# Performance work log

Hardware: AMD Instinct MI355X
Metric: run time of the kernel (lower is better)

## Reference

```python
import jax, jax.numpy as jnp
import numpy as np

N = 6720      # 16 graphs * 420 nodes
E = 33600     # 16 graphs * 2100 edges (5 per node)
DIN = 2048
H1, C1 = 2, 1024   # conv1: heads=2, out=1024 -> concat 2048
H2, C2 = 1, 64     # conv2: heads=1, out=64
ED = 64            # edge_dim
NODES_PER_GRAPH = 420


def _lin(k, fi, fo):
    return jax.random.normal(k, (fi, fo), jnp.float32) / np.sqrt(fi).astype(np.float32)


def setup_inputs() -> dict:
    key = jax.random.key(0)
    ks = jax.random.split(key, 24)
    d = {}
    d["x"] = jax.random.normal(ks[0], (N, DIN), jnp.float32)
    d["edge_index"] = jax.random.randint(ks[1], (2, E), 0, N)
    # tiled learned edge_features param (torch.rand init), one 2100xED block per graph
    ef = jax.random.uniform(ks[2], (5 * NODES_PER_GRAPH, ED), jnp.float32)
    d["edge_attr"] = jnp.tile(ef, (N // NODES_PER_GRAPH, 1))
    HC1 = H1 * C1
    d["q1_w"] = _lin(ks[3], DIN, HC1); d["q1_b"] = jax.random.normal(ks[4], (HC1,)) * 0.01
    d["k1_w"] = _lin(ks[5], DIN, HC1); d["k1_b"] = jax.random.normal(ks[6], (HC1,)) * 0.01
    d["v1_w"] = _lin(ks[7], DIN, HC1); d["v1_b"] = jax.random.normal(ks[8], (HC1,)) * 0.01
    d["e1_w"] = _lin(ks[9], ED, HC1)                      # lin_edge has no bias in PyG
    d["s1_w"] = _lin(ks[10], DIN, HC1); d["s1_b"] = jax.random.normal(ks[11], (HC1,)) * 0.01
    HC2 = H2 * C2
    d["q2_w"] = _lin(ks[12], HC1, HC2); d["q2_b"] = jax.random.normal(ks[13], (HC2,)) * 0.01
    d["k2_w"] = _lin(ks[14], HC1, HC2); d["k2_b"] = jax.random.normal(ks[15], (HC2,)) * 0.01
    d["v2_w"] = _lin(ks[16], HC1, HC2); d["v2_b"] = jax.random.normal(ks[17], (HC2,)) * 0.01
    d["e2_w"] = _lin(ks[18], ED, HC2)
    d["s2_w"] = _lin(ks[19], HC1, HC2); d["s2_b"] = jax.random.normal(ks[20], (HC2,)) * 0.01
    return d


def _transformer_conv(x, src, dst, edge_attr, qw, qb, kw, kb, vw, vb, ew, sw, sb, H, C):
    """PyG TransformerConv (concat=True, beta=False, root_weight=True)."""
    n = x.shape[0]
    q = (x @ qw + qb).reshape(n, H, C)
    k = (x @ kw + kb).reshape(n, H, C)
    v = (x @ vw + vb).reshape(n, H, C)
    e = (edge_attr @ ew).reshape(-1, H, C)         # [E,H,C]
    kj = k[src] + e                                # gather source keys + edge emb
    alpha = jnp.sum(q[dst] * kj, axis=-1) / np.sqrt(C).astype(np.float32)  # [E,H]
    # scatter-softmax over incoming edges of each target node
    amax = jax.ops.segment_max(alpha, dst, num_segments=n)   # [N,H]
    ex = jnp.exp(alpha - amax[dst])
    denom = jax.ops.segment_sum(ex, dst, num_segments=n)
    attn = ex / (denom[dst] + 1e-16)               # [E,H]
    msg = (v[src] + e) * attn[..., None]           # [E,H,C]
    out = jax.ops.segment_sum(msg, dst, num_segments=n).reshape(n, H * C)
    return out + x @ sw + sb                       # root/skip connection


def reference(x, edge_index, edge_attr,
              q1_w, q1_b, k1_w, k1_b, v1_w, v1_b, e1_w, s1_w, s1_b,
              q2_w, q2_b, k2_w, k2_b, v2_w, v2_b, e2_w, s2_w, s2_b):
    src, dst = edge_index[0], edge_index[1]
    h = jax.nn.relu(_transformer_conv(x, src, dst, edge_attr,
                                      q1_w, q1_b, k1_w, k1_b, v1_w, v1_b,
                                      e1_w, s1_w, s1_b, H1, C1))
    h = jax.nn.relu(_transformer_conv(h, src, dst, edge_attr,
                                      q2_w, q2_b, k2_w, k2_b, v2_w, v2_b,
                                      e2_w, s2_w, s2_b, H2, C2))
    return h.reshape(-1, NODES_PER_GRAPH * 64)     # forward returns here (fc layers are dead code)
```

## Files before the change

### kernel.cpp

```cpp
#include <hip/hip_runtime.h>
#include <hip/hip_bf16.h>
#include <cstdint>
#include <cstddef>

#define NN    6720
#define MPAD  6912
#define NE    33600
#define KDIM  2048
#define HC1   2048
#define EAP   2100

typedef __attribute__((ext_vector_type(8))) short bhalf8;
typedef __attribute__((ext_vector_type(4))) short bhalf4;
typedef __attribute__((ext_vector_type(4))) float fx4;

__device__ __forceinline__ float bf2f(short s) {
    union { unsigned int u; float f; } c;
    c.u = ((unsigned int)(unsigned short)s) << 16;
    return c.f;
}

__device__ __forceinline__ void gload16(const __hip_bfloat16* g, void* lds)
{
    __builtin_amdgcn_global_load_lds(
        (const __attribute__((address_space(1))) unsigned int*)g,
        (__attribute__((address_space(3))) unsigned int*)lds,
        16, 0, 0);
}

#define CFENCE asm volatile("" ::: "memory")

__global__ __launch_bounds__(512, 2) void gemm256_8ph(
    const __hip_bfloat16* __restrict__ A,
    const __hip_bfloat16* __restrict__ Bt,
    const float* __restrict__ bcat,
    __hip_bfloat16* __restrict__ oq,
    __hip_bfloat16* __restrict__ ok,
    __hip_bfloat16* __restrict__ ov,
    float* __restrict__ oh)
{
    __shared__ alignas(16) char Lds[131072];

    const int bid = blockIdx.x;
    const int i0  = bid >> 3;
    const int bx  = (bid & 7) * 4 + (i0 & 3);
    const int by  = i0 >> 2;

    const int tid  = threadIdx.x;
    const int w    = tid >> 6;
    const int lane = tid & 63;
    const int wm = w >> 2, wn = w & 3;
    const int l15 = lane & 15;
    const int rowA = by * 256;
    const int rowB = bx * 256;

    const int sug = ((lane & 7) ^ (lane >> 3)) << 3;
    const __hip_bfloat16* Agb = A  + (size_t)(rowA + w * 16 + (lane >> 3)) * KDIM + sug;
    const __hip_bfloat16* Bgb = Bt + (size_t)(rowB + w * 16 + (lane >> 3)) * KDIM + sug;

    const int uk0 = (((lane >> 4)    ) ^ (lane & 7)) << 4;
    const int uk1 = (((lane >> 4) + 4) ^ (lane & 7)) << 4;

    fx4 acc[8][4] = {};

#define STAGE_A(T, H)                                                      \
    { char* dst_ = Lds + ((T) & 1) * 32768 + (H) * 16384 + (w * 16) * 128; \
      const __hip_bfloat16* g_ = Agb + (size_t)((H) * 128) * KDIM + (size_t)(T) * 64; \
      gload16(g_, dst_);                                                   \
      gload16(g_ + 8 * KDIM, dst_ + 1024); }

#define STAGE_B(T, H)                                                      \
    { char* dst_ = Lds + 65536 + ((T) & 1) * 32768 + (H) * 16384 + (w * 16) * 128; \
      const __hip_bfloat16* g_ = Bgb + (size_t)((H) * 128) * KDIM + (size_t)(T) * 64; \
      gload16(g_, dst_);                                                   \
      gload16(g_ + 8 * KDIM, dst_ + 1024); }

#define PH_READ_AF(q)                                                      \
    _Pragma("unroll")                                                      \
    for (int m2 = 0; m2 < 2; ++m2) {                                       \
        const char* rp_ = Ab + (((q) * 2 + m2) * 16 + l15) * 128;          \
        af[m2][0] = *(const bhalf8*)(rp_ + uk0);                           \
        af[m2][1] = *(const bhalf8*)(rp_ + uk1);                           \
    }

#define PH_MFMA(q)                                                         \
    __builtin_amdgcn_s_setprio(1);                                         \
    _Pragma("unroll")                                                      \
    for (int m2 = 0; m2 < 2; ++m2)                                         \
        _Pragma("unroll")                                                  \
        for (int nj = 0; nj < 4; ++nj)                                     \
            _Pragma("unroll")                                              \
            for (int kk = 0; kk < 2; ++kk)                                 \
                acc[(q) * 2 + m2][nj] = __builtin_amdgcn_mfma_f32_16x16x32_bf16( \
                    af[m2][kk], bf[nj][kk], acc[(q) * 2 + m2][nj], 0, 0, 0); \
    __builtin_amdgcn_s_setprio(0);

    STAGE_A(0, 0); STAGE_B(0, 0); STAGE_A(0, 1); STAGE_B(0, 1);

    for (int T = 0; T < 32; ++T) {
        const char* Ab = Lds + (T & 1) * 32768 + wm * 16384;
        const char* Bb = Lds + 65536 + (T & 1) * 32768 + (wn >> 1) * 16384;
        bhalf8 bf[4][2], af[2][2];

        if (T < 31) { STAGE_A(T + 1, 0); }
        if (T < 31) { asm volatile("s_waitcnt vmcnt(2)" ::: "memory"); }
        else        { asm volatile("s_waitcnt vmcnt(0)" ::: "memory"); }
        __builtin_amdgcn_s_barrier(); CFENCE;
        #pragma unroll
        for (int nj = 0; nj < 4; ++nj) {
            const char* rp_ = Bb + ((wn & 1) * 64 + nj * 16 + l15) * 128;
            bf[nj][0] = *(const bhalf8*)(rp_ + uk0);
            bf[nj][1] = *(const bhalf8*)(rp_ + uk1);
        }
        PH_READ_AF(0);
        PH_MFMA(0);
        CFENCE; __builtin_amdgcn_s_barrier(); CFENCE;
        if (T < 31) { STAGE_B(T + 1, 0); }
        PH_READ_AF(1);
        PH_MFMA(1);
        CFENCE; __builtin_amdgcn_s_barrier(); CFENCE;
        if (T < 31) { STAGE_A(T + 1, 1); }
        PH_READ_AF(2);
        PH_MFMA(2);
        CFENCE; __builtin_amdgcn_s_barrier(); CFENCE;
        if (T < 31) { STAGE_B(T + 1, 1); }
        PH_READ_AF(3);
        PH_MFMA(3);
        CFENCE; __builtin_amdgcn_s_barrier(); CFENCE;
    }
#undef PH_MFMA
#undef PH_READ_AF
#undef STAGE_B
#undef STAGE_A

    const int gcol = rowB + wn * 64;
    const int seg  = gcol >> 11;
    const int lcol = gcol & 2047;
    float bv[4];
    #pragma unroll
    for (int nj = 0; nj < 4; ++nj) bv[nj] = bcat[gcol + nj * 16 + l15];
    char* scr = Lds + w * 8704;
    const int growA = rowA + wm * 128;

    #pragma unroll
    for (int c = 0; c < 4; ++c) {
        #pragma unroll
        for (int m2 = 0; m2 < 2; ++m2) {
            const int mi = c * 2 + m2;
            #pragma unroll
            for (int nj = 0; nj < 4; ++nj) {
                const int cl = nj * 16 + l15;
                #pragma unroll
                for (int i2 = 0; i2 < 4; ++i2) {
                    const int rl = m2 * 16 + ((lane >> 4) << 2) + i2;
                    *(float*)(scr + rl * 272 + cl * 4) = acc[mi][nj][i2] + bv[nj];
                }
            }
        }
        asm volatile("s_waitcnt lgkmcnt(0)" ::: "memory");
        CFENCE;
        const int rrow = (lane >> 4);
        const int u    = lane & 15;
        if (seg < 3) {
            __hip_bfloat16* dst = (seg == 0) ? oq : (seg == 1) ? ok : ov;
            #pragma unroll
            for (int p = 0; p < 8; ++p) {
                const int row = p * 4 + rrow;
                const float4 f = *(const float4*)(scr + row * 272 + u * 16);
                bhalf4 tb;
                tb[0] = (short)__bfloat16_as_ushort(__float2bfloat16(f.x));
                tb[1] = (short)__bfloat16_as_ushort(__float2bfloat16(f.y));
                tb[2] = (short)__bfloat16_as_ushort(__float2bfloat16(f.z));
                tb[3] = (short)__bfloat16_as_ushort(__float2bfloat16(f.w));
                *(bhalf4*)&dst[(size_t)(growA + c * 32 + row) * 2048 + lcol + u * 4] = tb;
            }
        } else {
            #pragma unroll
            for (int p = 0; p < 8; ++p) {
                const int row = p * 4 + rrow;
                const float4 f = *(const float4*)(scr + row * 272 + u * 16);
                *(float4*)&oh[(size_t)(growA + c * 32 + row) * 2048 + lcol + u * 4] = f;
            }
        }
        asm volatile("s_waitcnt lgkmcnt(0)" ::: "memory");
        CFENCE;
    }
}

__global__ __launch_bounds__(256) void gemm_bf16(
    const __hip_bfloat16* __restrict__ A,
    const __hip_bfloat16* __restrict__ Bt,
    const float* __restrict__ bias,
    float* __restrict__ C,
    __hip_bfloat16* __restrict__ Cb,
    int M, int N, int K, int flags)
{
    __shared__ alignas(16) __hip_bfloat16 Asm[128 * 64];
    __shared__ alignas(16) __hip_bfloat16 Bsm[128 * 64];
    const int tid  = threadIdx.x;
    const int w    = tid >> 6;
    const int lane = tid & 63;
    const int wr = w >> 1, wc = w & 1;
    const int rowA = blockIdx.y * 128;
    const int rowB = blockIdx.x * 128;
    const int klen = K / gridDim.z;
    const int kbeg = blockIdx.z * klen;

    const int srow = w * 32 + (lane >> 3);
    const int ug8  = ((lane & 7) ^ (lane >> 3)) << 3;
    const __hip_bfloat16* Ag = A  + (size_t)(rowA + srow) * K + ug8;
    const __hip_bfloat16* Bg = Bt + (size_t)(rowB + srow) * K + ug8;
    char* AsBase = (char*)Asm + w * 4096;
    char* BsBase = (char*)Bsm + w * 4096;

    fx4 acc[4][4] = {};

    const int fra = wr * 64 + (lane & 15);
    const int frb = wc * 64 + (lane & 15);
    const int kb  = (lane >> 4) << 4;
    const int swz = (lane & 7) << 4;

    for (int k0 = kbeg; k0 < kbeg + klen; k0 += 64) {
        __syncthreads();
        #pragma unroll
        for (int j = 0; j < 4; ++j) {
            gload16(Ag + (size_t)j * 8 * K + k0, AsBase + j * 1024);
            gload16(Bg + (size_t)j * 8 * K + k0, BsBase + j * 1024);
        }
        __syncthreads();
        #pragma unroll
        for (int kk = 0; kk < 2; ++kk) {
            const int cb = kk * 64 + kb;
            bhalf8 af[4], bfr[4];
            #pragma unroll
            for (int mi = 0; mi < 4; ++mi)
                af[mi] = *(const bhalf8*)((const char*)Asm + (fra + mi * 16) * 128 + (cb ^ swz));
            #pragma unroll
            for (int nj = 0; nj < 4; ++nj)
                bfr[nj] = *(const bhalf8*)((const char*)Bsm + (frb + nj * 16) * 128 + (cb ^ swz));
            #pragma unroll
            for (int mi = 0; mi < 4; ++mi)
                #pragma unroll
                for (int nj = 0; nj < 4; ++nj)
                    acc[mi][nj] = __builtin_amdgcn_mfma_f32_16x16x32_bf16(
                        af[mi], bfr[nj], acc[mi][nj], 0, 0, 0);
        }
    }

    float* Cz = C ? C + (size_t)blockIdx.z * ((size_t)M * N) : nullptr;
    #pragma unroll
    for (int nj = 0; nj < 4; ++nj) {
        const int ccol = rowB + wc * 64 + nj * 16 + (lane & 15);
        const float bv = (flags & 1) ? bias[ccol] : 0.f;
        #pragma unroll
        for (int mi = 0; mi < 4; ++mi) {
            const int crow0 = rowA + wr * 64 + mi * 16 + ((lane >> 4) << 2);
            #pragma unroll
            for (int i = 0; i < 4; ++i) {
                size_t idx = (size_t)(crow0 + i) * N + ccol;
                float v = acc[mi][nj][i] + bv;
                if (flags & 2) v += Cz[idx];
                if (flags & 4) v = fmaxf(v, 0.f);
                if (Cz && !(flags & 8)) Cz[idx] = v;
                if (Cb) Cb[idx] = __float2bfloat16(v);
            }
        }
    }
}

__global__ void reduce4(const float* __restrict__ parts, size_t stride,
                        const float* __restrict__ bias, int colmask,
                        float* __restrict__ dst, int n)
{
    int i = blockIdx.x * 256 + threadIdx.x;
    if (i >= n) return;
    float v = parts[i] + parts[stride + i] + parts[2 * stride + i] + parts[3 * stride + i];
    if (bias) v += bias[i & colmask];
    dst[i] = v;
}

__global__ __launch_bounds__(256) void gemm_tile(
    const float* __restrict__ A, const float* __restrict__ B,
    const float* __restrict__ bias, float* __restrict__ C,
    int M, int N, int K, int flags)
{
    __shared__ float As[16][68];
    __shared__ float Bs[16][64];
    const int tid = threadIdx.x;
    const int bx = blockIdx.x, by = blockIdx.y;
    const int tx = tid & 15, ty = tid >> 4;
    const int arow = tid >> 2, acol = (tid & 3) << 2;
    const int brow = tid >> 4, bcol = (tid & 15) << 2;
    const float* Ag = A + (size_t)(by * 64 + arow) * K + acol;
    const float* Bg = B + (size_t)brow * N + bx * 64 + bcol;
    float acc[4][4] = {};
    for (int k0 = 0; k0 < K; k0 += 16) {
        const float4 av = *(const float4*)(Ag + k0);
        const float4 bv = *(const float4*)(Bg + (size_t)k0 * N);
        __syncthreads();
        As[acol + 0][arow] = av.x;
        As[acol + 1][arow] = av.y;
        As[acol + 2][arow] = av.z;
        As[acol + 3][arow] = av.w;
        *(float4*)&Bs[brow][bcol] = bv;
        __syncthreads();
        #pragma unroll
        for (int kk = 0; kk < 16; ++kk) {
            const float4 a4 = *(const float4*)&As[kk][ty << 2];
            const float4 b4 = *(const float4*)&Bs[kk][tx << 2];
            const float a[4] = {a4.x, a4.y, a4.z, a4.w};
            const float b[4] = {b4.x, b4.y, b4.z, b4.w};
            #pragma unroll
            for (int i = 0; i < 4; ++i)
                #pragma unroll
                for (int j = 0; j < 4; ++j)
                    acc[i][j] += a[i] * b[j];
        }
    }
    const int crow = by * 64 + (ty << 2);
    const int ccol = bx * 64 + (tx << 2);
    float4 b4 = make_float4(0.f, 0.f, 0.f, 0.f);
    if (flags & 1) b4 = *(const float4*)(bias + ccol);
    #pragma unroll
    for (int i = 0; i < 4; ++i) {
        float* cp = C + (size_t)(crow + i) * N + ccol;
        float4 v;
        v.x = acc[i][0] + b4.x; v.y = acc[i][1] + b4.y;
        v.z = acc[i][2] + b4.z; v.w = acc[i][3] + b4.w;
        if (flags & 2) {
            const float4 o = *(const float4*)cp;
            v.x += o.x; v.y += o.y; v.z += o.z; v.w += o.w;
        }
        *(float4*)cp = v;
    }
}

__global__ void count_deg(const int* __restrict__ ei, int* __restrict__ deg)
{
    int e = blockIdx.x * 256 + threadIdx.x;
    if (e < NE) atomicAdd(&deg[ei[NE + e]], 1);
}

__global__ __launch_bounds__(1024) void scan_kernel(const int* __restrict__ deg,
                                                    int* __restrict__ rowptr)
{
    __shared__ int s[1024];
    const int t = threadIdx.x;
    const int base = t * 7;
    int loc[7];
    int sum = 0;
    #pragma unroll
    for (int i = 0; i < 7; ++i) {
        int idx = base + i;
        int v = (idx < NN) ? deg[idx] : 0;
        loc[i] = v; sum += v;
    }
    s[t] = sum;
    __syncthreads();
    for (int off = 1; off < 1024; off <<= 1) {
        int v = (t >= off) ? s[t - off] : 0;
        __syncthreads();
        s[t] += v;
        __syncthreads();
    }
    int running = s[t] - sum;
    #pragma unroll
    for (int i = 0; i < 7; ++i) {
        int idx = base + i;
        if (idx <= NN) rowptr[idx] = running;
        if (idx < NN) running += loc[i];
    }
}

__global__ void fill_csr(const int* __restrict__ ei, const int* __restrict__ rowptr,
                         int* __restrict__ fillctr, int* __restrict__ elist)
{
    int e = blockIdx.x * 256 + threadIdx.x;
    if (e >= NE) return;
    int d = ei[NE + e];
    int pos = atomicAdd(&fillctr[d], 1);
    elist[rowptr[d] + pos] = e;
}

__global__ void sort_csr(const int* __restrict__ rowptr, int* __restrict__ elist)
{
    int n = blockIdx.x * 256 + threadIdx.x;
    if (n >= NN) return;
    int s0 = rowptr[n], s1 = rowptr[n + 1];
    for (int i = s0 + 1; i < s1; ++i) {
        int v = elist[i];
        int j = i - 1;
        while (j >= s0 && elist[j] > v) { elist[j + 1] = elist[j]; --j; }
        elist[j + 1] = v;
    }
}

__global__ void cvt_pad_bf16(const float* __restrict__ src, __hip_bfloat16* __restrict__ dst,
                             int relu)
{
    size_t i = (size_t)(blockIdx.x * 256 + threadIdx.x) * 4;
    int row = (int)(i >> 11);
    float4 v = make_float4(0.f, 0.f, 0.f, 0.f);
    if (row < NN) v = *(const float4*)&src[i];
    if (relu) {
        v.x = fmaxf(v.x, 0.f); v.y = fmaxf(v.y, 0.f);
        v.z = fmaxf(v.z, 0.f); v.w = fmaxf(v.w, 0.f);
    }
    dst[i + 0] = __float2bfloat16(v.x);
    dst[i + 1] = __float2bfloat16(v.y);
    dst[i + 2] = __float2bfloat16(v.z);
    dst[i + 3] = __float2bfloat16(v.w);
}

__global__ __launch_bounds__(256) void transpose_cvt4(
    const float* __restrict__ W0, const float* __restrict__ W1,
    const float* __restrict__ W2, const float* __restrict__ W3,
    __hip_bfloat16* __restrict__ dst)
{
    const float* W = (blockIdx.z == 0) ? W0 : (blockIdx.z == 1) ? W1
                   : (blockIdx.z == 2) ? W2 : W3;
    __hip_bfloat16* Bt = dst + (size_t)blockIdx.z * KDIM * KDIM;
    __shared__ float t[32][33];
    int kb = blockIdx.y * 32, nb = blockIdx.x * 32;
    int tx = threadIdx.x & 31, ty = threadIdx.x >> 5;
    #pragma unroll
    for (int i = 0; i < 32; i += 8)
        t[ty + i][tx] = W[(size_t)(kb + ty + i) * KDIM + nb + tx];
    __syncthreads();
    #pragma unroll
    for (int i = 0; i < 32; i += 8)
        Bt[(size_t)(nb + ty + i) * KDIM + kb + tx] = __float2bfloat16(t[tx][ty + i]);
}

__global__ void build_bcat(const float* __restrict__ q1b, const float* __restrict__ k1b,
                           const float* __restrict__ v1b, const float* __restrict__ s1b,
                           float* __restrict__ bcat)
{
    int i = blockIdx.x * 256 + threadIdx.x;
    if (i >= 4 * KDIM) return;
    int seg = i >> 11, j = i & 2047;
    const float* b = (seg == 0) ? q1b : (seg == 1) ? k1b : (seg == 2) ? v1b : s1b;
    bcat[i] = b[j];
}

__global__ void build_w1pp(const float* __restrict__ e1w, __hip_bfloat16* __restrict__ w1pp)
{
    int idx = blockIdx.x * 256 + threadIdx.x;
    int p = idx >> 11, j = idx & 2047;
    float v = ((j >> 10) == (p >> 6)) ? e1w[(size_t)(p & 63) * KDIM + j] : 0.f;
    w1pp[idx] = __float2bfloat16(v);
}

__global__ void build_w1ppT(const float* __restrict__ e1w, __hip_bfloat16* __restrict__ w1ppT)
{
    int idx = blockIdx.x * 256 + threadIdx.x;
    int n = idx >> 7, k = idx & 127;
    float v = ((n >> 10) == (k >> 6)) ? e1w[(size_t)(k & 63) * KDIM + n] : 0.f;
    w1ppT[idx] = __float2bfloat16(v);
}

__global__ void build_w2t(const float* __restrict__ qw, const float* __restrict__ kw,
                          const float* __restrict__ vw, const float* __restrict__ sw,
                          const float* __restrict__ qb, const float* __restrict__ kb,
                          const float* __restrict__ vb, const float* __restrict__ sb,
                          __hip_bfloat16* __restrict__ w2t, float* __restrict__ b2)
{
    int idx = blockIdx.x * 256 + threadIdx.x;
    int c = idx >> 11, d = idx & 2047;
    int g = c >> 6, j = c & 63;
    const float* w = (g == 0) ? qw : (g == 1) ? kw : (g == 2) ? vw : sw;
    w2t[idx] = __float2bfloat16(w[(size_t)d * 64 + j]);
    if (d == 0) {
        const float* b = (g == 0) ? qb : (g == 1) ? kb : (g == 2) ? vb : sb;
        b2[c] = b[j];
    }
}

__global__ __launch_bounds__(256) void node1_kernel(
    const __hip_bfloat16* __restrict__ q1b, const __hip_bfloat16* __restrict__ k1b,
    const __hip_bfloat16* __restrict__ v1b,
    const float* __restrict__ P1, const float* __restrict__ ea,
    const int* __restrict__ ei, const int* __restrict__ rowptr,
    const int* __restrict__ elist,
    float* __restrict__ h1, __hip_bfloat16* __restrict__ R1)
{
    __shared__ int   s_src[256];
    __shared__ int   s_em[256];
    __shared__ float s_at[256][2];
    const int n = blockIdx.x;
    const int s0 = rowptr[n];
    const int deg = rowptr[n + 1] - s0;
    const int w = threadIdx.x >> 6, lane = threadIdx.x & 63;

    for (int j = w; j < deg; j += 4) {
        const int e = elist[s0 + j];
        const int src = ei[e];
        const int em = e % EAP;
        if (lane == 0) { s_src[j] = src; s_em[j] = em; }
        const float eaj = ea[(size_t)em * 64 + lane];
        #pragma unroll
        for (int h = 0; h < 2; ++h) {
            const __hip_bfloat16* qh = q1b + (size_t)n * HC1 + h * 1024 + lane * 16;
            const __hip_bfloat16* kh = k1b + (size_t)src * HC1 + h * 1024 + lane * 16;
            bhalf8 qa = *(const bhalf8*)qh, qc = *(const bhalf8*)(qh + 8);
            bhalf8 ka = *(const bhalf8*)kh, kc = *(const bhalf8*)(kh + 8);
            float s = 0.f;
            #pragma unroll
            for (int jj = 0; jj < 8; ++jj) s += bf2f(qa[jj]) * bf2f(ka[jj]);
            #pragma unroll
            for (int jj = 0; jj < 8; ++jj) s += bf2f(qc[jj]) * bf2f(kc[jj]);
            s += eaj * P1[(size_t)n * 128 + h * 64 + lane];
            #pragma unroll
            for (int off = 32; off; off >>= 1) s += __shfl_xor(s, off);
            if (lane == 0) s_at[j][h] = s * 0.03125f;
        }
    }
    __syncthreads();

    if (threadIdx.x < 2) {
        const int h = threadIdx.x;
        float m = -1e30f;
        for (int j = 0; j < deg; ++j) m = fmaxf(m, s_at[j][h]);
        float sum = 0.f;
        for (int j = 0; j < deg; ++j) {
            float ex = __expf(s_at[j][h] - m);
            s_at[j][h] = ex; sum += ex;
        }
        float inv = 1.f / (sum + 1e-16f);
        for (int j = 0; j < deg; ++j) s_at[j][h] *= inv;
    }
    __syncthreads();

    if (threadIdx.x < 128) {
        const int h = threadIdx.x >> 6, jj = threadIdx.x & 63;
        float r = 0.f;
        for (int j = 0; j < deg; ++j)
            r += s_at[j][h] * ea[(size_t)s_em[j] * 64 + jj];
        R1[(size_t)n * 128 + threadIdx.x] = __float2bfloat16(r);
    }

    const int c0 = threadIdx.x * 8;
    const int h = c0 >> 10;
    float acc[8];
    const float4 p0 = *(const float4*)&h1[(size_t)n * HC1 + c0];
    const float4 p1 = *(const float4*)&h1[(size_t)n * HC1 + c0 + 4];
    acc[0] = p0.x; acc[1] = p0.y; acc[2] = p0.z; acc[3] = p0.w;
    acc[4] = p1.x; acc[5] = p1.y; acc[6] = p1.z; acc[7] = p1.w;
    for (int j = 0; j < deg; ++j) {
        const float at = s_at[j][h];
        bhalf8 v = *(const bhalf8*)&v1b[(size_t)s_src[j] * HC1 + c0];
        #pragma unroll
        for (int jj = 0; jj < 8; ++jj) acc[jj] += at * bf2f(v[jj]);
    }
    *(float4*)&h1[(size_t)n * HC1 + c0]     = make_float4(acc[0], acc[1], acc[2], acc[3]);
    *(float4*)&h1[(size_t)n * HC1 + c0 + 4] = make_float4(acc[4], acc[5], acc[6], acc[7]);
}

__global__ __launch_bounds__(64) void node2_kernel(
    const float* __restrict__ qkvs2, const float* __restrict__ E2s,
    const int* __restrict__ ei, const int* __restrict__ rowptr,
    const int* __restrict__ elist, float* __restrict__ out)
{
    __shared__ float s_at[256];
    __shared__ int   s_src[256];
    __shared__ int   s_em[256];
    const int n = blockIdx.x;
    const int s0 = rowptr[n];
    const int deg = rowptr[n + 1] - s0;
    const int c = threadIdx.x;
    const float q = qkvs2[(size_t)n * 256 + c];

    for (int j = 0; j < deg; ++j) {
        const int e = elist[s0 + j];
        const int src = ei[e];
        const int em = e % EAP;
        float s = q * (qkvs2[(size_t)src * 256 + 64 + c] + E2s[(size_t)em * 64 + c]);
        #pragma unroll
        for (int off = 32; off; off >>= 1) s += __shfl_xor(s, off);
        if (c == 0) { s_at[j] = s * 0.125f; s_src[j] = src; s_em[j] = em; }
    }
    __syncthreads();
    float m = -1e30f;
    for (int j = 0; j < deg; ++j) m = fmaxf(m, s_at[j]);
    float sum = 0.f;
    for (int j = 0; j < deg; ++j) sum += __expf(s_at[j] - m);
    const float inv = 1.f / (sum + 1e-16f);

    float acc = qkvs2[(size_t)n * 256 + 192 + c];
    for (int j = 0; j < deg; ++j) {
        const float at = __expf(s_at[j] - m) * inv;
        acc += at * (qkvs2[(size_t)s_src[j] * 256 + 128 + c] + E2s[(size_t)s_em[j] * 64 + c]);
    }
    out[(size_t)n * 64 + c] = fmaxf(acc, 0.f);
}

extern "C" void kernel_launch(void* const* d_in, const int* in_sizes, int n_in,
                              void* d_out, int out_size, void* d_ws, size_t ws_size,
                              hipStream_t stream)
{
    const float* x   = (const float*)d_in[0];
    const int*   ei  = (const int*)d_in[1];
    const float* ea  = (const float*)d_in[2];
    const float* q1w = (const float*)d_in[3];
    const float* q1b = (const float*)d_in[4];
    const float* k1w = (const float*)d_in[5];
    const float* k1b = (const float*)d_in[6];
    const float* v1w = (const float*)d_in[7];
    const float* v1b = (const float*)d_in[8];
    const float* e1w = (const float*)d_in[9];
    const float* s1w = (const float*)d_in[10];
    const float* s1b = (const float*)d_in[11];
    const float* q2w = (const float*)d_in[12];
    const float* q2b = (const float*)d_in[13];
    const float* k2w = (const float*)d_in[14];
    const float* k2b = (const float*)d_in[15];
    const float* v2w = (const float*)d_in[16];
    const float* v2b = (const float*)d_in[17];
    const float* e2w = (const float*)d_in[18];
    const float* s2w = (const float*)d_in[19];
    const float* s2b = (const float*)d_in[20];
    float* out = (float*)d_out;

    char* base = (char*)d_ws;
    size_t off = 0;
    auto alloc = [&](size_t nbytes) {
        size_t o = off; off += (nbytes + 255) & ~(size_t)255; return o;
    };
    const size_t xb_off   = alloc((size_t)MPAD * KDIM * 2);
    const size_t wcat_off = alloc((size_t)4 * KDIM * KDIM * 2);
    __hip_bfloat16* xb    = (__hip_bfloat16*)(base + xb_off);
    __hip_bfloat16* wcat  = (__hip_bfloat16*)(base + wcat_off);
    __hip_bfloat16* h1b   = xb;
    float*          Cpart = (float*)(base + wcat_off);
    __hip_bfloat16* w2t   = (__hip_bfloat16*)(base + wcat_off + (size_t)29 * 1024 * 1024);

    __hip_bfloat16* q1bb  = (__hip_bfloat16*)(base + alloc((size_t)MPAD * HC1 * 2));
    __hip_bfloat16* k1bb  = (__hip_bfloat16*)(base + alloc((size_t)MPAD * HC1 * 2));
    __hip_bfloat16* v1bb  = (__hip_bfloat16*)(base + alloc((size_t)MPAD * HC1 * 2));
    float*          h1    = (float*)(base + alloc((size_t)MPAD * HC1 * 4));
    float*          bcat  = (float*)(base + alloc((size_t)4 * KDIM * 4));
    float*          P1    = (float*)(base + alloc((size_t)MPAD * 128 * 4));
    __hip_bfloat16* R1b   = (__hip_bfloat16*)(base + alloc((size_t)MPAD * 128 * 2));
    __hip_bfloat16* w1pp  = (__hip_bfloat16*)(base + alloc((size_t)128 * KDIM * 2));
    __hip_bfloat16* w1ppT = (__hip_bfloat16*)(base + alloc((size_t)KDIM * 128 * 2));
    float*          b2    = (float*)(base + alloc(256 * 4));
    float*          qkvs2 = (float*)(base + alloc((size_t)MPAD * 256 * 4));
    float*          E2s   = (float*)(base + alloc((size_t)2112 * 64 * 4));
    int* deg    = (int*)(base + alloc((size_t)NN * 4));
    int* fill   = (int*)(base + alloc((size_t)NN * 4));
    int* rowptr = (int*)(base + alloc((size_t)(NN + 1) * 4));
    int* elist  = (int*)(base + alloc((size_t)NE * 4));

    hipMemsetAsync(deg, 0, sizeof(int) * 2 * NN, stream);
    count_deg<<<(NE + 255) / 256, 256, 0, stream>>>(ei, deg);
    scan_kernel<<<1, 1024, 0, stream>>>(deg, rowptr);
    fill_csr<<<(NE + 255) / 256, 256, 0, stream>>>(ei, rowptr, fill, elist);
    sort_csr<<<(NN + 255) / 256, 256, 0, stream>>>(rowptr, elist);

    const int cvblk = (MPAD * KDIM / 4) / 256;
    cvt_pad_bf16<<<cvblk, 256, 0, stream>>>(x, xb, 0);
    transpose_cvt4<<<dim3(KDIM / 32, KDIM / 32, 4), 256, 0, stream>>>(q1w, k1w, v1w, s1w, wcat);
    build_bcat<<<(4 * KDIM) / 256, 256, 0, stream>>>(q1b, k1b, v1b, s1b, bcat);
    build_w1pp<<<(128 * KDIM) / 256, 256, 0, stream>>>(e1w, w1pp);
    build_w1ppT<<<(KDIM * 128) / 256, 256, 0, stream>>>(e1w, w1ppT);
    gemm_tile<<<dim3(1, 33), 256, 0, stream>>>(ea, e2w, nullptr, E2s, 2112, 64, 64, 0);

    gemm256_8ph<<<864, 512, 0, stream>>>(xb, wcat, bcat, q1bb, k1bb, v1bb, h1);

    gemm_bf16<<<dim3(1, MPAD / 128, 4), 256, 0, stream>>>(q1bb, w1pp, nullptr, Cpart, nullptr,
                                                          MPAD, 128, KDIM, 0);
    reduce4<<<(MPAD * 128) / 256, 256, 0, stream>>>(Cpart, (size_t)MPAD * 128, nullptr, 0,
                                                    P1, MPAD * 128);

    node1_kernel<<<NN, 256, 0, stream>>>(q1bb, k1bb, v1bb, P1, ea, ei, rowptr, elist, h1, R1b);
    gemm_bf16<<<dim3(HC1 / 128, MPAD / 128), 256, 0, stream>>>(R1b, w1ppT, nullptr, h1, h1b,
                                                               MPAD, HC1, 128, 2 | 4 | 8);

    build_w2t<<<(256 * KDIM) / 256, 256, 0, stream>>>(q2w, k2w, v2w, s2w, q2b, k2b, v2b, s2b,
                                                      w2t, b2);
    gemm_bf16<<<dim3(2, MPAD / 128, 4), 256, 0, stream>>>(h1b, w2t, nullptr, Cpart, nullptr,
                                                          MPAD, 256, KDIM, 0);
    reduce4<<<(MPAD * 256) / 256, 256, 0, stream>>>(Cpart, (size_t)MPAD * 256, b2, 255,
                                                    qkvs2, MPAD * 256);

    node2_kernel<<<NN, 64, 0, stream>>>(qkvs2, E2s, ei, rowptr, elist, out);

    (void)in_sizes; (void)n_in; (void)out_size; (void)ws_size;
}
```

Baseline: 483.4 us.

## Restructure main GEMM LDS layout and pipeline, merge weight-prep kernels

Reworks the main 256x256 bf16 GEMM so the LDS tile is split into two 32-wide K halves with a new swizzle. All A/B fragments for a K-step are read up front, and global-to-LDS staging is issued two iterations ahead, interleaved with four MFMA quarters. It also merges the bcat, w1pp, w1ppT and w2t preparation kernels into a single launch, with w2t moved to its own buffer. The aim is better overlap of global loads with MFMA work and fewer kernel launches, at the cost of more fragment registers and tighter vmcnt bookkeeping.

```diff
diff --git a/kernel.cpp b/kernel.cpp
--- a/kernel.cpp
+++ b/kernel.cpp
@@ -30,7 +30,7 @@
 
 #define CFENCE asm volatile("" ::: "memory")
 
-__global__ __launch_bounds__(512, 2) void gemm256_8ph(
+__global__ __launch_bounds__(512, 2) void gemm256_fl(
     const __hip_bfloat16* __restrict__ A,
     const __hip_bfloat16* __restrict__ Bt,
     const float* __restrict__ bcat,
@@ -54,84 +54,75 @@
     const int rowA = by * 256;
     const int rowB = bx * 256;
 
-    const int sug = ((lane & 7) ^ (lane >> 3)) << 3;
-    const __hip_bfloat16* Agb = A  + (size_t)(rowA + w * 16 + (lane >> 3)) * KDIM + sug;
-    const __hip_bfloat16* Bgb = Bt + (size_t)(rowB + w * 16 + (lane >> 3)) * KDIM + sug;
-
-    const int uk0 = (((lane >> 4)    ) ^ (lane & 7)) << 4;
-    const int uk1 = (((lane >> 4) + 4) ^ (lane & 7)) << 4;
+    const int sug = ((lane & 3) ^ ((lane >> 3) & 3)) << 3;
+    const __hip_bfloat16* Agb = A  + (size_t)(rowA + w * 32 + (lane >> 2)) * KDIM + sug;
+    const __hip_bfloat16* Bgb = Bt + (size_t)(rowB + w * 32 + (lane >> 2)) * KDIM + sug;
+
+    const int rds = ((lane >> 4) ^ ((l15 >> 1) & 3)) << 4;
 
     fx4 acc[8][4] = {};
 
-#define STAGE_A(T, H)                                                      \
-    { char* dst_ = Lds + ((T) & 1) * 32768 + (H) * 16384 + (w * 16) * 128; \
-      const __hip_bfloat16* g_ = Agb + (size_t)((H) * 128) * KDIM + (size_t)(T) * 64; \
+#define STAGE(TS, H)                                                       \
+    { char* dst_ = Lds + (((H) >> 1) ? 65536 : 0) + ((TS) & 1) * 32768     \
+                   + ((H) & 1) * 16384 + w * 2048;                         \
+      const __hip_bfloat16* g_ = ((((H) >> 1)) ? Bgb : Agb)                \
+                   + (size_t)(TS) * 64 + ((H) & 1) * 32;                   \
       gload16(g_, dst_);                                                   \
-      gload16(g_ + 8 * KDIM, dst_ + 1024); }
-
-#define STAGE_B(T, H)                                                      \
-    { char* dst_ = Lds + 65536 + ((T) & 1) * 32768 + (H) * 16384 + (w * 16) * 128; \
-      const __hip_bfloat16* g_ = Bgb + (size_t)((H) * 128) * KDIM + (size_t)(T) * 64; \
-      gload16(g_, dst_);                                                   \
-      gload16(g_ + 8 * KDIM, dst_ + 1024); }
-
-#define PH_READ_AF(q)                                                      \
-    _Pragma("unroll")                                                      \
-    for (int m2 = 0; m2 < 2; ++m2) {                                       \
-        const char* rp_ = Ab + (((q) * 2 + m2) * 16 + l15) * 128;          \
-        af[m2][0] = *(const bhalf8*)(rp_ + uk0);                           \
-        af[m2][1] = *(const bhalf8*)(rp_ + uk1);                           \
-    }
-
-#define PH_MFMA(q)                                                         \
+      gload16(g_ + 16 * KDIM, dst_ + 1024); }
+
+#define QMFMA(MI0, KK)                                                     \
     __builtin_amdgcn_s_setprio(1);                                         \
     _Pragma("unroll")                                                      \
-    for (int m2 = 0; m2 < 2; ++m2)                                         \
+    for (int mi = 0; mi < 4; ++mi)                                         \
         _Pragma("unroll")                                                  \
         for (int nj = 0; nj < 4; ++nj)                                     \
-            _Pragma("unroll")                                              \
-            for (int kk = 0; kk < 2; ++kk)                                 \
-                acc[(q) * 2 + m2][nj] = __builtin_amdgcn_mfma_f32_16x16x32_bf16( \
-                    af[m2][kk], bf[nj][kk], acc[(q) * 2 + m2][nj], 0, 0, 0); \
+            acc[(MI0) + mi][nj] = __builtin_amdgcn_mfma_f32_16x16x32_bf16( \
+                af[(MI0) + mi][KK], bf[nj][KK], acc[(MI0) + mi][nj], 0, 0, 0); \
     __builtin_amdgcn_s_setprio(0);
 
-    STAGE_A(0, 0); STAGE_B(0, 0); STAGE_A(0, 1); STAGE_B(0, 1);
+    STAGE(0, 0); STAGE(0, 1); STAGE(0, 2); STAGE(0, 3);
+    STAGE(1, 0); STAGE(1, 1); STAGE(1, 2);
+    asm volatile("s_waitcnt vmcnt(6)" ::: "memory");
+    __builtin_amdgcn_s_barrier(); CFENCE;
 
     for (int T = 0; T < 32; ++T) {
-        const char* Ab = Lds + (T & 1) * 32768 + wm * 16384;
-        const char* Bb = Lds + 65536 + (T & 1) * 32768 + (wn >> 1) * 16384;
-        bhalf8 bf[4][2], af[2][2];
-
-        if (T < 31) { STAGE_A(T + 1, 0); }
-        if (T < 31) { asm volatile("s_waitcnt vmcnt(2)" ::: "memory"); }
-        else        { asm volatile("s_waitcnt vmcnt(0)" ::: "memory"); }
-        __builtin_amdgcn_s_barrier(); CFENCE;
-        #pragma unroll
-        for (int nj = 0; nj < 4; ++nj) {
-            const char* rp_ = Bb + ((wn & 1) * 64 + nj * 16 + l15) * 128;
-            bf[nj][0] = *(const bhalf8*)(rp_ + uk0);
-            bf[nj][1] = *(const bhalf8*)(rp_ + uk1);
-        }
-        PH_READ_AF(0);
-        PH_MFMA(0);
+        const char* A0 = Lds + (T & 1) * 32768;
+        const char* B0 = Lds + 65536 + (T & 1) * 32768;
+        bhalf8 af[8][2], bf[4][2];
+
+        #pragma unroll
+        for (int nj = 0; nj < 4; ++nj)
+            bf[nj][0] = *(const bhalf8*)(B0 + (wn * 64 + nj * 16 + l15) * 64 + rds);
+        #pragma unroll
+        for (int mi = 0; mi < 8; ++mi)
+            af[mi][0] = *(const bhalf8*)(A0 + (wm * 128 + mi * 16 + l15) * 64 + rds);
+        #pragma unroll
+        for (int nj = 0; nj < 4; ++nj)
+            bf[nj][1] = *(const bhalf8*)(B0 + 16384 + (wn * 64 + nj * 16 + l15) * 64 + rds);
+        #pragma unroll
+        for (int mi = 0; mi < 8; ++mi)
+            af[mi][1] = *(const bhalf8*)(A0 + 16384 + (wm * 128 + mi * 16 + l15) * 64 + rds);
+        if (T <= 30) { STAGE(T + 1, 3) }
+        CFENCE;
+        __builtin_amdgcn_s_barrier();
+        asm volatile("s_waitcnt lgkmcnt(0)" ::: "memory");
+        CFENCE;
+        QMFMA(0, 0)
         CFENCE; __builtin_amdgcn_s_barrier(); CFENCE;
-        if (T < 31) { STAGE_B(T + 1, 0); }
-        PH_READ_AF(1);
-        PH_MFMA(1);
+        if (T <= 29) { STAGE(T + 2, 0) }
+        QMFMA(4, 0)
         CFENCE; __builtin_amdgcn_s_barrier(); CFENCE;
-        if (T < 31) { STAGE_A(T + 1, 1); }
-        PH_READ_AF(2);
-        PH_MFMA(2);
+        if (T <= 29) { STAGE(T + 2, 1) }
+        QMFMA(0, 1)
         CFENCE; __builtin_amdgcn_s_barrier(); CFENCE;
-        if (T < 31) { STAGE_B(T + 1, 1); }
-        PH_READ_AF(3);
-        PH_MFMA(3);
+        if (T <= 29) { STAGE(T + 2, 2) }
+        QMFMA(4, 1)
+        if (T <= 29)      { asm volatile("s_waitcnt vmcnt(6)" ::: "memory"); }
+        else if (T == 30) { asm volatile("s_waitcnt vmcnt(0)" ::: "memory"); }
         CFENCE; __builtin_amdgcn_s_barrier(); CFENCE;
     }
-#undef PH_MFMA
-#undef PH_READ_AF
-#undef STAGE_B
-#undef STAGE_A
+#undef QMFMA
+#undef STAGE
 
     const int gcol = rowB + wn * 64;
     const int seg  = gcol >> 11;
@@ -432,46 +423,46 @@
         Bt[(size_t)(nb + ty + i) * KDIM + kb + tx] = __float2bfloat16(t[tx][ty + i]);
 }
 
-__global__ void build_bcat(const float* __restrict__ q1b, const float* __restrict__ k1b,
-                           const float* __restrict__ v1b, const float* __restrict__ s1b,
-                           float* __restrict__ bcat)
-{
-    int i = blockIdx.x * 256 + threadIdx.x;
-    if (i >= 4 * KDIM) return;
-    int seg = i >> 11, j = i & 2047;
-    const float* b = (seg == 0) ? q1b : (seg == 1) ? k1b : (seg == 2) ? v1b : s1b;
-    bcat[i] = b[j];
-}
-
-__global__ void build_w1pp(const float* __restrict__ e1w, __hip_bfloat16* __restrict__ w1pp)
+__global__ void build_misc(
+    const float* __restrict__ q1b, const float* __restrict__ k1b,
+    const float* __restrict__ v1b, const float* __restrict__ s1b,
+    const float* __restrict__ e1w,
+    const float* __restrict__ q2w, const float* __restrict__ k2w,
+    const float* __restrict__ v2w, const float* __restrict__ s2w,
+    const float* __restrict__ q2bb, const float* __restrict__ k2bb,
+    const float* __restrict__ v2bb, const float* __restrict__ s2bb,
+    float* __restrict__ bcat, __hip_bfloat16* __restrict__ w1pp,
+    __hip_bfloat16* __restrict__ w1ppT, __hip_bfloat16* __restrict__ w2t,
+    float* __restrict__ b2)
 {
     int idx = blockIdx.x * 256 + threadIdx.x;
-    int p = idx >> 11, j = idx & 2047;
-    float v = ((j >> 10) == (p >> 6)) ? e1w[(size_t)(p & 63) * KDIM + j] : 0.f;
-    w1pp[idx] = __float2bfloat16(v);
-}
-
-__global__ void build_w1ppT(const float* __restrict__ e1w, __hip_bfloat16* __restrict__ w1ppT)
-{
-    int idx = blockIdx.x * 256 + threadIdx.x;
-    int n = idx >> 7, k = idx & 127;
-    float v = ((n >> 10) == (k >> 6)) ? e1w[(size_t)(k & 63) * KDIM + n] : 0.f;
-    w1ppT[idx] = __float2bfloat16(v);
-}
-
-__global__ void build_w2t(const float* __restrict__ qw, const float* __restrict__ kw,
-                          const float* __restrict__ vw, const float* __restrict__ sw,
-                          const float* __restrict__ qb, const float* __restrict__ kb,
-                          const float* __restrict__ vb, const float* __restrict__ sb,
-                          __hip_bfloat16* __restrict__ w2t, float* __restrict__ b2)
-{
-    int idx = blockIdx.x * 256 + threadIdx.x;
+    if (idx < 8192) {
+        int seg = idx >> 11, j = idx & 2047;
+        const float* b = (seg == 0) ? q1b : (seg == 1) ? k1b : (seg == 2) ? v1b : s1b;
+        bcat[idx] = b[j];
+        return;
+    }
+    idx -= 8192;
+    if (idx < 262144) {
+        int p = idx >> 11, j = idx & 2047;
+        float v = ((j >> 10) == (p >> 6)) ? e1w[(size_t)(p & 63) * KDIM + j] : 0.f;
+        w1pp[idx] = __float2bfloat16(v);
+        return;
+    }
+    idx -= 262144;
+    if (idx < 262144) {
+        int n = idx >> 7, k = idx & 127;
+        float v = ((n >> 10) == (k >> 6)) ? e1w[(size_t)(k & 63) * KDIM + n] : 0.f;
+        w1ppT[idx] = __float2bfloat16(v);
+        return;
+    }
+    idx -= 262144;
     int c = idx >> 11, d = idx & 2047;
     int g = c >> 6, j = c & 63;
-    const float* w = (g == 0) ? qw : (g == 1) ? kw : (g == 2) ? vw : sw;
+    const float* w = (g == 0) ? q2w : (g == 1) ? k2w : (g == 2) ? v2w : s2w;
     w2t[idx] = __float2bfloat16(w[(size_t)d * 64 + j]);
     if (d == 0) {
-        const float* b = (g == 0) ? qb : (g == 1) ? kb : (g == 2) ? vb : sb;
+        const float* b = (g == 0) ? q2bb : (g == 1) ? k2bb : (g == 2) ? v2bb : s2bb;
         b2[c] = b[j];
     }
 }
@@ -632,7 +623,6 @@
     __hip_bfloat16* wcat  = (__hip_bfloat16*)(base + wcat_off);
     __hip_bfloat16* h1b   = xb;
     float*          Cpart = (float*)(base + wcat_off);
-    __hip_bfloat16* w2t   = (__hip_bfloat16*)(base + wcat_off + (size_t)29 * 1024 * 1024);
 
     __hip_bfloat16* q1bb  = (__hip_bfloat16*)(base + alloc((size_t)MPAD * HC1 * 2));
     __hip_bfloat16* k1bb  = (__hip_bfloat16*)(base + alloc((size_t)MPAD * HC1 * 2));
@@ -643,6 +633,7 @@
     __hip_bfloat16* R1b   = (__hip_bfloat16*)(base + alloc((size_t)MPAD * 128 * 2));
     __hip_bfloat16* w1pp  = (__hip_bfloat16*)(base + alloc((size_t)128 * KDIM * 2));
     __hip_bfloat16* w1ppT = (__hip_bfloat16*)(base + alloc((size_t)KDIM * 128 * 2));
+    __hip_bfloat16* w2t   = (__hip_bfloat16*)(base + alloc((size_t)256 * KDIM * 2));
     float*          b2    = (float*)(base + alloc(256 * 4));
     float*          qkvs2 = (float*)(base + alloc((size_t)MPAD * 256 * 4));
     float*          E2s   = (float*)(base + alloc((size_t)2112 * 64 * 4));
@@ -660,12 +651,12 @@
     const int cvblk = (MPAD * KDIM / 4) / 256;
     cvt_pad_bf16<<<cvblk, 256, 0, stream>>>(x, xb, 0);
     transpose_cvt4<<<dim3(KDIM / 32, KDIM / 32, 4), 256, 0, stream>>>(q1w, k1w, v1w, s1w, wcat);
-    build_bcat<<<(4 * KDIM) / 256, 256, 0, stream>>>(q1b, k1b, v1b, s1b, bcat);
-    build_w1pp<<<(128 * KDIM) / 256, 256, 0, stream>>>(e1w, w1pp);
-    build_w1ppT<<<(KDIM * 128) / 256, 256, 0, stream>>>(e1w, w1ppT);
+    build_misc<<<4128, 256, 0, stream>>>(q1b, k1b, v1b, s1b, e1w,
+                                         q2w, k2w, v2w, s2w, q2b, k2b, v2b, s2b,
+                                         bcat, w1pp, w1ppT, w2t, b2);
     gemm_tile<<<dim3(1, 33), 256, 0, stream>>>(ea, e2w, nullptr, E2s, 2112, 64, 64, 0);
 
-    gemm256_8ph<<<864, 512, 0, stream>>>(xb, wcat, bcat, q1bb, k1bb, v1bb, h1);
+    gemm256_fl<<<864, 512, 0, stream>>>(xb, wcat, bcat, q1bb, k1bb, v1bb, h1);
 
     gemm_bf16<<<dim3(1, MPAD / 128, 4), 256, 0, stream>>>(q1bb, w1pp, nullptr, Cpart, nullptr,
                                                           MPAD, 128, KDIM, 0);
@@ -676,8 +667,6 @@
     gemm_bf16<<<dim3(HC1 / 128, MPAD / 128), 256, 0, stream>>>(R1b, w1ppT, nullptr, h1, h1b,
                                                                MPAD, HC1, 128, 2 | 4 | 8);
 
-    build_w2t<<<(256 * KDIM) / 256, 256, 0, stream>>>(q2w, k2w, v2w, s2w, q2b, k2b, v2b, s2b,
-                                                      w2t, b2);
     gemm_bf16<<<dim3(2, MPAD / 128, 4), 256, 0, stream>>>(h1b, w2t, nullptr, Cpart, nullptr,
                                                           MPAD, 256, KDIM, 0);
     reduce4<<<(MPAD * 256) / 256, 256, 0, stream>>>(Cpart, (size_t)MPAD * 256, b2, 255,
```

Result: no change. 477.5 us (-1.2%).
